# Kernel tuning notes

Measured on AMD Instinct MI355X. Metric: run time of the kernel, lower is better.

## Reference

```python
import jax, jax.numpy as jnp
import numpy as np

TOTAL = 819200   # total flattened labels
BATCH = 16384    # number of samples (segments)
DIM = 128        # embed_dim
LABELS_PER = 50  # constant segment length (TOTAL = BATCH * LABELS_PER)


def setup_inputs() -> dict:
    key = jax.random.key(0)
    k_emb, k_w1, k_b1, k_w2, k_b2 = jax.random.split(key, 5)
    embeddings = jax.random.normal(k_emb, (TOTAL, DIM), dtype=jnp.float32)
    # weight_net params (PyTorch nn.Linear default-ish init scale)
    s1 = 1.0 / np.sqrt(DIM)
    W1 = jax.random.uniform(k_w1, (DIM, DIM), jnp.float32, -s1, s1)
    b1 = jax.random.uniform(k_b1, (DIM,), jnp.float32, -s1, s1)
    W2 = jax.random.uniform(k_w2, (DIM, 1), jnp.float32, -s1, s1)
    b2 = jax.random.uniform(k_b2, (1,), jnp.float32, -s1, s1)
    lengths = jnp.full((BATCH,), LABELS_PER, dtype=jnp.int32)
    return {"embeddings": embeddings, "W1": W1, "b1": b1, "W2": W2, "b2": b2,
            "lengths": lengths}


def reference(embeddings, W1, b1, W2, b2, lengths):
    # MLP scorer: Linear -> ReLU -> Linear -> Softmax(dim=0) (GLOBAL over all labels)
    h = jnp.maximum(embeddings @ W1 + b1, 0.0)           # (T, D)
    scores = h @ W2 + b2                                  # (T, 1)
    weights = jax.nn.softmax(scores, axis=0)              # (T, 1) global softmax
    # Ragged per-segment weighted sum via segment_sum
    batch = lengths.shape[0]
    total = embeddings.shape[0]
    seg_ids = jnp.repeat(jnp.arange(batch, dtype=jnp.int32), lengths,
                         total_repeat_length=total)       # (T,)
    pooled = jax.ops.segment_sum(embeddings * weights, seg_ids,
                                 num_segments=batch)      # (B, D)
    return pooled
```

## Files before the change

### kernel.cpp

```cpp
#include <hip/hip_runtime.h>
#include <hip/hip_bf16.h>
#include <math.h>

#define DIM 128

typedef __attribute__((ext_vector_type(8))) short bf16x8;
typedef __attribute__((ext_vector_type(4))) float f32x4;

union FragU { bf16x8 v; __hip_bfloat162 h[4]; };

static __device__ __forceinline__ ushort f2bf(float f) {
    unsigned u = __float_as_uint(f);
    u += 0x7FFFu + ((u >> 16) & 1u);
    return (ushort)(u >> 16);
}

typedef __attribute__((address_space(1))) const unsigned GASp;
typedef __attribute__((address_space(3))) unsigned LASp;
static __device__ __forceinline__ void gll16(const void* g, void* l) {
    __builtin_amdgcn_global_load_lds((GASp*)g, (LASp*)l, 16, 0, 0);
}

static __device__ __forceinline__ void stage16(float* buf, const float* emb,
                                               long row0, long Tm1, int lane) {
    #pragma unroll
    for (int i = 0; i < 8; ++i) {
        int s = i * 64 + lane;
        int r = s >> 5, x = s & 31;
        long gr = row0 + r; gr = (gr > Tm1) ? Tm1 : gr;
        gll16(emb + gr * 128 + ((x ^ (r & 7)) << 2), (char*)buf + i * 1024);
    }
}

__global__ __launch_bounds__(1024) void scan_kernel(const int* __restrict__ lengths,
                                                    int* __restrict__ offsets, int batch) {
    __shared__ int tsum[1024];
    int tid = threadIdx.x;
    int per = (batch + 1023) >> 10;
    int start = tid * per;
    int s = 0;
    for (int i = 0; i < per; ++i) {
        int idx = start + i;
        if (idx < batch) s += lengths[idx];
    }
    tsum[tid] = s;
    __syncthreads();
    for (int off = 1; off < 1024; off <<= 1) {
        int v = (tid >= off) ? tsum[tid - off] : 0;
        __syncthreads();
        tsum[tid] += v;
        __syncthreads();
    }
    int base = (tid == 0) ? 0 : tsum[tid - 1];
    for (int i = 0; i < per; ++i) {
        int idx = start + i;
        if (idx < batch) { offsets[idx] = base; base += lengths[idx]; }
    }
}

__global__ __launch_bounds__(256, 2) void fused_kernel(
        const float* __restrict__ emb, const float* __restrict__ W1,
        const float* __restrict__ b1, const float* __restrict__ W2,
        const float* __restrict__ b2, const int* __restrict__ offsets,
        const int* __restrict__ lengths, int batch, int T,
        float* __restrict__ mArr, float* __restrict__ sArr,
        float* __restrict__ tvec) {
    __shared__ __align__(16) char smem[65536];

    int tid = threadIdx.x;
    int lane = tid & 63;
    int wv = tid >> 6;
    int lr = lane & 15;
    int lg = lane >> 4;

    ushort* sB = (ushort*)smem;
    for (int i = 0; i < 16; ++i) {
        int q = tid + i * 256;
        int n = q >> 5;
        int k4 = q & 31;
        ushort4 w;
        w.x = f2bf(W1[(k4 * 4 + 0) * DIM + n]);
        w.y = f2bf(W1[(k4 * 4 + 1) * DIM + n]);
        w.z = f2bf(W1[(k4 * 4 + 2) * DIM + n]);
        w.w = f2bf(W1[(k4 * 4 + 3) * DIM + n]);
        int c = k4 >> 1;
        int a16 = n * 128 + ((c ^ (n & 7)) * 8) + (k4 & 1) * 4;
        *(ushort4*)&sB[a16] = w;
    }
    __syncthreads();
    bf16x8 bfrag[8][4];
    #pragma unroll
    for (int ct = 0; ct < 8; ++ct) {
        int n = ct * 16 + lr;
        #pragma unroll
        for (int kc = 0; kc < 4; ++kc) {
            int c = lg + kc * 4;
            bfrag[ct][kc] = *(const bf16x8*)&sB[n * 128 + ((c ^ (n & 7)) * 8)];
        }
    }
    float b1reg[8], w2reg[8];
    #pragma unroll
    for (int ct = 0; ct < 8; ++ct) {
        b1reg[ct] = b1[ct * 16 + lr];
        w2reg[ct] = W2[ct * 16 + lr];
    }
    __syncthreads();

    float* buf0 = (float*)(smem + wv * 16384);
    float* buf1 = (float*)(smem + wv * 16384 + 8192);

    long Tm1 = (long)T - 1;
    int nwaves = gridDim.x * 4;
    int gwave = blockIdx.x * 4 + wv;
    int per = (batch + nwaves - 1) / nwaves;
    int seg0 = gwave * per;
    int segend = seg0 + per; if (segend > batch) segend = batch;

    for (int seg = seg0; seg < segend; ++seg) {
        long off = offsets[seg];
        int len = lengths[seg];
        int nch = (len + 15) >> 4;
        float r_ref = -INFINITY, Sp = 0.f, t0 = 0.f, t1 = 0.f;

        if (nch > 0) stage16(buf0, emb, off, Tm1, lane);
        if (nch > 1) stage16(buf1, emb, off + 16, Tm1, lane);

        for (int c = 0; c < nch; ++c) {
            float* bufc = (c & 1) ? buf1 : buf0;
            if (c + 1 < nch) asm volatile("s_waitcnt vmcnt(8)" ::: "memory");
            else             asm volatile("s_waitcnt vmcnt(0)" ::: "memory");

            bf16x8 a[4];
            #pragma unroll
            for (int kc = 0; kc < 4; ++kc) {
                int c0 = kc * 8 + lg * 2;
                float4 q0 = *(const float4*)&bufc[(lr * 32 + (c0 ^ (lr & 7))) * 4];
                float4 q1 = *(const float4*)&bufc[(lr * 32 + ((c0 + 1) ^ (lr & 7))) * 4];
                FragU f;
                f.h[0] = __float22bfloat162_rn(make_float2(q0.x, q0.y));
                f.h[1] = __float22bfloat162_rn(make_float2(q0.z, q0.w));
                f.h[2] = __float22bfloat162_rn(make_float2(q1.x, q1.y));
                f.h[3] = __float22bfloat162_rn(make_float2(q1.z, q1.w));
                a[kc] = f.v;
            }

            asm volatile("s_waitcnt lgkmcnt(0)" ::: "memory");
            if (c + 2 < nch) stage16(bufc, emb, off + (long)(c + 2) * 16, Tm1, lane);

            f32x4 acc[8];
            #pragma unroll
            for (int ct = 0; ct < 8; ++ct) acc[ct] = (f32x4)(0.f);
            #pragma unroll
            for (int ct = 0; ct < 8; ++ct)
                #pragma unroll
                for (int kc = 0; kc < 4; ++kc)
                    acc[ct] = __builtin_amdgcn_mfma_f32_16x16x32_bf16(a[kc], bfrag[ct][kc], acc[ct], 0, 0, 0);

            float p[4];
            #pragma unroll
            for (int reg = 0; reg < 4; ++reg) {
                float s = 0.f;
                #pragma unroll
                for (int ct = 0; ct < 8; ++ct) {
                    float h = acc[ct][reg] + b1reg[ct];
                    h = fmaxf(h, 0.f);
                    s = fmaf(h, w2reg[ct], s);
                }
                p[reg] = s;
            }
            #pragma unroll
            for (int m = 1; m < 16; m <<= 1) {
                #pragma unroll
                for (int reg = 0; reg < 4; ++reg)
                    p[reg] += __shfl_xor(p[reg], m, 64);
            }
            int r3 = lane & 3;
            float pr = p[0];
            pr = (r3 == 1) ? p[1] : pr;
            pr = (r3 == 2) ? p[2] : pr;
            pr = (r3 == 3) ? p[3] : pr;
            int src = ((lane & 12) << 2) + r3;
            float sv = __shfl(pr, src, 64);

            int cv = len - c * 16;
            float s_l = (lr < cv) ? sv : -INFINITY;

            if (!__all(s_l - r_ref <= 8.f)) {
                float m_c = s_l;
                #pragma unroll
                for (int o = 1; o < 16; o <<= 1) m_c = fmaxf(m_c, __shfl_xor(m_c, o, 64));
                float r_new = fmaxf(r_ref, m_c);
                float scl = __expf(r_ref - r_new);
                Sp *= scl; t0 *= scl; t1 *= scl;
                r_ref = r_new;
            }
            float w_l = __expf(s_l - r_ref);
            Sp += w_l;

            long rbase = off + (long)c * 16;
            #pragma unroll
            for (int j = 0; j < 16; ++j) {
                long prow = rbase + j; prow = (prow > Tm1) ? Tm1 : prow;
                float wj = __uint_as_float(__builtin_amdgcn_readlane(__float_as_uint(w_l), j));
                float2 e = *(const float2*)(emb + prow * 128 + 2 * lane);
                t0 = fmaf(wj, e.x, t0);
                t1 = fmaf(wj, e.y, t1);
            }
        }

        #pragma unroll
        for (int o = 1; o < 16; o <<= 1) Sp += __shfl_xor(Sp, o, 64);
        *(float2*)&tvec[(long)seg * DIM + 2 * lane] = make_float2(t0, t1);
        if (lane == 0) { mArr[seg] = r_ref; sArr[seg] = Sp; }
    }
}

__global__ __launch_bounds__(1024) void segreduce_kernel(const float* __restrict__ mArr,
        const float* __restrict__ sArr, int batch, float* __restrict__ stats) {
    __shared__ float redm[16], reds[16];
    int tid = threadIdx.x;
    int wave = tid >> 6, ln = tid & 63;
    float m = -INFINITY;
    for (int i = tid; i < batch; i += 1024) m = fmaxf(m, mArr[i]);
    #pragma unroll
    for (int o = 32; o >= 1; o >>= 1) m = fmaxf(m, __shfl_xor(m, o, 64));
    if (ln == 0) redm[wave] = m;
    __syncthreads();
    float M = -INFINITY;
    #pragma unroll
    for (int k = 0; k < 16; ++k) M = fmaxf(M, redm[k]);
    float s = 0.f;
    for (int i = tid; i < batch; i += 1024) s += sArr[i] * expf(mArr[i] - M);
    #pragma unroll
    for (int o = 32; o >= 1; o >>= 1) s += __shfl_xor(s, o, 64);
    if (ln == 0) reds[wave] = s;
    __syncthreads();
    if (tid == 0) {
        float S = 0.f;
        #pragma unroll
        for (int k = 0; k < 16; ++k) S += reds[k];
        stats[0] = M;
        stats[1] = 1.0f / S;
    }
}

__global__ __launch_bounds__(256) void scale_kernel(const float* __restrict__ tvec,
        const float* __restrict__ mArr, const float* __restrict__ stats,
        float* __restrict__ out, int n) {
    int idx = blockIdx.x * 256 + threadIdx.x;
    if (idx >= n) return;
    float M = stats[0], invS = stats[1];
    int b = idx >> 7;
    out[idx] = tvec[idx] * (expf(mArr[b] - M) * invS);
}

extern "C" void kernel_launch(void* const* d_in, const int* in_sizes, int n_in,
                              void* d_out, int out_size, void* d_ws, size_t ws_size,
                              hipStream_t stream) {
    const float* emb     = (const float*)d_in[0];
    const float* W1      = (const float*)d_in[1];
    const float* b1      = (const float*)d_in[2];
    const float* W2      = (const float*)d_in[3];
    const float* b2      = (const float*)d_in[4];
    const int*   lengths = (const int*)d_in[5];
    int T = in_sizes[0] / DIM;
    int batch = in_sizes[5];
    float* out = (float*)d_out;

    int*   offsets = (int*)d_ws;
    float* mArr    = (float*)(offsets + batch);
    float* sArr    = mArr + batch;
    float* stats   = sArr + batch;
    float* tvec    = stats + 2;

    scan_kernel<<<1, 1024, 0, stream>>>(lengths, offsets, batch);
    fused_kernel<<<512, 256, 0, stream>>>(emb, W1, b1, W2, b2, offsets, lengths,
                                          batch, T, mArr, sArr, tvec);
    segreduce_kernel<<<1, 1024, 0, stream>>>(mArr, sArr, batch, stats);
    scale_kernel<<<(out_size + 255) / 256, 256, 0, stream>>>(tvec, mArr, stats, out, out_size);
}
```

Baseline: 188.0 us.

## Replace LDS staging with register prefetch and read W1 fragments from LDS

Drops the per-wave LDS double buffer filled by global_load_lds and instead prefetches the next 16-row chunk of embeddings straight into registers. W1 bf16 fragments are now read from a 32KB shared array inside the MFMA loop rather than held in registers, which frees registers and LDS. The kernel asks for three blocks per CU and the grid doubles to 1024 blocks. The weighted-sum loop gains a fast path for full chunks and an exact-length tail loop, so the clamp on T is gone. The cost is extra LDS traffic per MFMA and register-based prefetch depth in place of asynchronous LDS fills.

```diff
diff --git a/kernel.cpp b/kernel.cpp
--- a/kernel.cpp
+++ b/kernel.cpp
@@ -13,23 +13,6 @@
     unsigned u = __float_as_uint(f);
     u += 0x7FFFu + ((u >> 16) & 1u);
     return (ushort)(u >> 16);
-}
-
-typedef __attribute__((address_space(1))) const unsigned GASp;
-typedef __attribute__((address_space(3))) unsigned LASp;
-static __device__ __forceinline__ void gll16(const void* g, void* l) {
-    __builtin_amdgcn_global_load_lds((GASp*)g, (LASp*)l, 16, 0, 0);
-}
-
-static __device__ __forceinline__ void stage16(float* buf, const float* emb,
-                                               long row0, long Tm1, int lane) {
-    #pragma unroll
-    for (int i = 0; i < 8; ++i) {
-        int s = i * 64 + lane;
-        int r = s >> 5, x = s & 31;
-        long gr = row0 + r; gr = (gr > Tm1) ? Tm1 : gr;
-        gll16(emb + gr * 128 + ((x ^ (r & 7)) << 2), (char*)buf + i * 1024);
-    }
 }
 
 __global__ __launch_bounds__(1024) void scan_kernel(const int* __restrict__ lengths,
@@ -58,14 +41,14 @@
     }
 }
 
-__global__ __launch_bounds__(256, 2) void fused_kernel(
+__global__ __launch_bounds__(256, 3) void fused_kernel(
         const float* __restrict__ emb, const float* __restrict__ W1,
         const float* __restrict__ b1, const float* __restrict__ W2,
         const float* __restrict__ b2, const int* __restrict__ offsets,
         const int* __restrict__ lengths, int batch, int T,
         float* __restrict__ mArr, float* __restrict__ sArr,
         float* __restrict__ tvec) {
-    __shared__ __align__(16) char smem[65536];
+    __shared__ ushort sB[16384];
 
     int tid = threadIdx.x;
     int lane = tid & 63;
@@ -73,7 +56,6 @@
     int lr = lane & 15;
     int lg = lane >> 4;
 
-    ushort* sB = (ushort*)smem;
     for (int i = 0; i < 16; ++i) {
         int q = tid + i * 256;
         int n = q >> 5;
@@ -87,29 +69,19 @@
         int a16 = n * 128 + ((c ^ (n & 7)) * 8) + (k4 & 1) * 4;
         *(ushort4*)&sB[a16] = w;
     }
-    __syncthreads();
-    bf16x8 bfrag[8][4];
+    float b1r[8], w2r[8];
     #pragma unroll
     for (int ct = 0; ct < 8; ++ct) {
-        int n = ct * 16 + lr;
-        #pragma unroll
-        for (int kc = 0; kc < 4; ++kc) {
-            int c = lg + kc * 4;
-            bfrag[ct][kc] = *(const bf16x8*)&sB[n * 128 + ((c ^ (n & 7)) * 8)];
-        }
-    }
-    float b1reg[8], w2reg[8];
-    #pragma unroll
-    for (int ct = 0; ct < 8; ++ct) {
-        b1reg[ct] = b1[ct * 16 + lr];
-        w2reg[ct] = W2[ct * 16 + lr];
-    }
-    __syncthreads();
-
-    float* buf0 = (float*)(smem + wv * 16384);
-    float* buf1 = (float*)(smem + wv * 16384 + 8192);
-
-    long Tm1 = (long)T - 1;
+        b1r[ct] = b1[ct * 16 + lr];
+        w2r[ct] = W2[ct * 16 + lr];
+    }
+    __syncthreads();
+
+    const ushort* bp0 = &sB[lr * 128 + (((lg + 0) ^ (lr & 7)) * 8)];
+    const ushort* bp1 = &sB[lr * 128 + (((lg + 4) ^ (lr & 7)) * 8)];
+    const ushort* bp2 = &sB[lr * 128 + (((lg + 8) ^ (lr & 7)) * 8)];
+    const ushort* bp3 = &sB[lr * 128 + (((lg + 12) ^ (lr & 7)) * 8)];
+
     int nwaves = gridDim.x * 4;
     int gwave = blockIdx.x * 4 + wv;
     int per = (batch + nwaves - 1) / nwaves;
@@ -122,39 +94,61 @@
         int nch = (len + 15) >> 4;
         float r_ref = -INFINITY, Sp = 0.f, t0 = 0.f, t1 = 0.f;
 
-        if (nch > 0) stage16(buf0, emb, off, Tm1, lane);
-        if (nch > 1) stage16(buf1, emb, off + 16, Tm1, lane);
+        float4 n0, n1, n2, n3, n4, n5, n6, n7;
+        {
+            int rr = lr; if (rr > len - 1) rr = len - 1;
+            const float4* ap = (const float4*)(emb + (off + rr) * 128) + lg * 2;
+            n0 = ap[0];  n1 = ap[1];  n2 = ap[8];  n3 = ap[9];
+            n4 = ap[16]; n5 = ap[17]; n6 = ap[24]; n7 = ap[25];
+        }
 
         for (int c = 0; c < nch; ++c) {
-            float* bufc = (c & 1) ? buf1 : buf0;
-            if (c + 1 < nch) asm volatile("s_waitcnt vmcnt(8)" ::: "memory");
-            else             asm volatile("s_waitcnt vmcnt(0)" ::: "memory");
-
             bf16x8 a[4];
-            #pragma unroll
-            for (int kc = 0; kc < 4; ++kc) {
-                int c0 = kc * 8 + lg * 2;
-                float4 q0 = *(const float4*)&bufc[(lr * 32 + (c0 ^ (lr & 7))) * 4];
-                float4 q1 = *(const float4*)&bufc[(lr * 32 + ((c0 + 1) ^ (lr & 7))) * 4];
+            {
                 FragU f;
-                f.h[0] = __float22bfloat162_rn(make_float2(q0.x, q0.y));
-                f.h[1] = __float22bfloat162_rn(make_float2(q0.z, q0.w));
-                f.h[2] = __float22bfloat162_rn(make_float2(q1.x, q1.y));
-                f.h[3] = __float22bfloat162_rn(make_float2(q1.z, q1.w));
-                a[kc] = f.v;
-            }
-
-            asm volatile("s_waitcnt lgkmcnt(0)" ::: "memory");
-            if (c + 2 < nch) stage16(bufc, emb, off + (long)(c + 2) * 16, Tm1, lane);
+                f.h[0] = __float22bfloat162_rn(make_float2(n0.x, n0.y));
+                f.h[1] = __float22bfloat162_rn(make_float2(n0.z, n0.w));
+                f.h[2] = __float22bfloat162_rn(make_float2(n1.x, n1.y));
+                f.h[3] = __float22bfloat162_rn(make_float2(n1.z, n1.w));
+                a[0] = f.v;
+                f.h[0] = __float22bfloat162_rn(make_float2(n2.x, n2.y));
+                f.h[1] = __float22bfloat162_rn(make_float2(n2.z, n2.w));
+                f.h[2] = __float22bfloat162_rn(make_float2(n3.x, n3.y));
+                f.h[3] = __float22bfloat162_rn(make_float2(n3.z, n3.w));
+                a[1] = f.v;
+                f.h[0] = __float22bfloat162_rn(make_float2(n4.x, n4.y));
+                f.h[1] = __float22bfloat162_rn(make_float2(n4.z, n4.w));
+                f.h[2] = __float22bfloat162_rn(make_float2(n5.x, n5.y));
+                f.h[3] = __float22bfloat162_rn(make_float2(n5.z, n5.w));
+                a[2] = f.v;
+                f.h[0] = __float22bfloat162_rn(make_float2(n6.x, n6.y));
+                f.h[1] = __float22bfloat162_rn(make_float2(n6.z, n6.w));
+                f.h[2] = __float22bfloat162_rn(make_float2(n7.x, n7.y));
+                f.h[3] = __float22bfloat162_rn(make_float2(n7.z, n7.w));
+                a[3] = f.v;
+            }
+
+            if (c + 1 < nch) {
+                int rb = (c + 1) * 16 + lr; if (rb > len - 1) rb = len - 1;
+                const float4* ap = (const float4*)(emb + (off + rb) * 128) + lg * 2;
+                n0 = ap[0];  n1 = ap[1];  n2 = ap[8];  n3 = ap[9];
+                n4 = ap[16]; n5 = ap[17]; n6 = ap[24]; n7 = ap[25];
+            }
 
             f32x4 acc[8];
             #pragma unroll
             for (int ct = 0; ct < 8; ++ct) acc[ct] = (f32x4)(0.f);
             #pragma unroll
-            for (int ct = 0; ct < 8; ++ct)
-                #pragma unroll
-                for (int kc = 0; kc < 4; ++kc)
-                    acc[ct] = __builtin_amdgcn_mfma_f32_16x16x32_bf16(a[kc], bfrag[ct][kc], acc[ct], 0, 0, 0);
+            for (int ct = 0; ct < 8; ++ct) {
+                bf16x8 bf0 = *(const bf16x8*)(bp0 + ct * 2048);
+                bf16x8 bf1 = *(const bf16x8*)(bp1 + ct * 2048);
+                bf16x8 bf2 = *(const bf16x8*)(bp2 + ct * 2048);
+                bf16x8 bf3 = *(const bf16x8*)(bp3 + ct * 2048);
+                acc[ct] = __builtin_amdgcn_mfma_f32_16x16x32_bf16(a[0], bf0, acc[ct], 0, 0, 0);
+                acc[ct] = __builtin_amdgcn_mfma_f32_16x16x32_bf16(a[1], bf1, acc[ct], 0, 0, 0);
+                acc[ct] = __builtin_amdgcn_mfma_f32_16x16x32_bf16(a[2], bf2, acc[ct], 0, 0, 0);
+                acc[ct] = __builtin_amdgcn_mfma_f32_16x16x32_bf16(a[3], bf3, acc[ct], 0, 0, 0);
+            }
 
             float p[4];
             #pragma unroll
@@ -162,9 +156,9 @@
                 float s = 0.f;
                 #pragma unroll
                 for (int ct = 0; ct < 8; ++ct) {
-                    float h = acc[ct][reg] + b1reg[ct];
+                    float h = acc[ct][reg] + b1r[ct];
                     h = fmaxf(h, 0.f);
-                    s = fmaf(h, w2reg[ct], s);
+                    s = fmaf(h, w2r[ct], s);
                 }
                 p[reg] = s;
             }
@@ -197,14 +191,31 @@
             float w_l = __expf(s_l - r_ref);
             Sp += w_l;
 
-            long rbase = off + (long)c * 16;
-            #pragma unroll
-            for (int j = 0; j < 16; ++j) {
-                long prow = rbase + j; prow = (prow > Tm1) ? Tm1 : prow;
-                float wj = __uint_as_float(__builtin_amdgcn_readlane(__float_as_uint(w_l), j));
-                float2 e = *(const float2*)(emb + prow * 128 + 2 * lane);
-                t0 = fmaf(wj, e.x, t0);
-                t1 = fmaf(wj, e.y, t1);
+            long r0 = off + (long)c * 16;
+            if (cv >= 16) {
+                const float* pb0 = emb + r0 * 128 + 2 * lane;
+                const float* pb8 = pb0 + 8 * 128;
+                #pragma unroll
+                for (int j = 0; j < 8; ++j) {
+                    float wj = __uint_as_float(__builtin_amdgcn_readlane(__float_as_uint(w_l), j));
+                    float2 e = *(const float2*)(pb0 + j * 128);
+                    t0 = fmaf(wj, e.x, t0);
+                    t1 = fmaf(wj, e.y, t1);
+                }
+                #pragma unroll
+                for (int j = 0; j < 8; ++j) {
+                    float wj = __uint_as_float(__builtin_amdgcn_readlane(__float_as_uint(w_l), j + 8));
+                    float2 e = *(const float2*)(pb8 + j * 128);
+                    t0 = fmaf(wj, e.x, t0);
+                    t1 = fmaf(wj, e.y, t1);
+                }
+            } else {
+                for (int j = 0; j < cv; ++j) {
+                    float wj = __uint_as_float(__builtin_amdgcn_readlane(__float_as_uint(w_l), j));
+                    float2 e = *(const float2*)(emb + (r0 + j) * 128 + 2 * lane);
+                    t0 = fmaf(wj, e.x, t0);
+                    t1 = fmaf(wj, e.y, t1);
+                }
             }
         }
 
@@ -274,8 +285,8 @@
     float* tvec    = stats + 2;
 
     scan_kernel<<<1, 1024, 0, stream>>>(lengths, offsets, batch);
-    fused_kernel<<<512, 256, 0, stream>>>(emb, W1, b1, W2, b2, offsets, lengths,
-                                          batch, T, mArr, sArr, tvec);
+    fused_kernel<<<1024, 256, 0, stream>>>(emb, W1, b1, W2, b2, offsets, lengths,
+                                           batch, T, mArr, sArr, tvec);
     segreduce_kernel<<<1, 1024, 0, stream>>>(mArr, sArr, batch, stats);
     scale_kernel<<<(out_size + 255) / 256, 256, 0, stream>>>(tvec, mArr, stats, out, out_size);
 }
```

Measured after the change: 522.7 us. +178.1%, slower.
